# Performance work log

Measured on AMD Instinct MI355X. Metric: run time of the kernel, lower is better.

The kernel has to match this reference:

```python
import jax, jax.numpy as jnp
import numpy as np

# DeepseekV2MOE config (DeepSeek-V2-Lite-like, scaled)
T, H, E, I, K = 1024, 1024, 64, 512, 6
G, TKG = 8, 3          # n_group, topk_group
N_SHARED = 2
C = 256
SCALE = 2.5            # routed_scaling_factor


def setup_inputs() -> dict:
    key = jax.random.key(0)
    ks = jax.random.split(key, 7)
    inv = lambda d: 1.0 / np.sqrt(d).astype(np.float32)
    return {
        "hidden_states": jax.random.normal(ks[0], (T, H), jnp.float32),
        "gate_w": jax.random.normal(ks[1], (H, E), jnp.float32) * inv(H),
        "e_bias": jax.random.normal(ks[2], (E,), jnp.float32) * 0.01,  # e_score_correction_bias (noaux_tc)
        "w_gate_up": jax.random.normal(ks[3], (E, H, 2 * I), jnp.float32) * inv(H),
        "w_down": jax.random.normal(ks[4], (E, I, H), jnp.float32) * inv(I),
        "ws_gate_up": jax.random.normal(ks[5], (H, 2 * I * N_SHARED), jnp.float32) * inv(H),
        "ws_down": jax.random.normal(ks[6], (I * N_SHARED, H), jnp.float32) * inv(I * N_SHARED),
    }


def _silu_and_mul(gu):
    g, u = jnp.split(gu, 2, axis=-1)
    return jax.nn.silu(g) * u


def _grouped_topk(logits, bias):
    # DeepSeek-V3 noaux_tc grouped top-k with sigmoid scoring.
    scores = jax.nn.sigmoid(logits)                              # [T,E] original scores
    s = scores + bias[None, :]                                   # bias-corrected scores for selection
    grp = s.reshape(-1, G, E // G)
    grp_score = jax.lax.top_k(grp, 2)[0].sum(-1)                 # [T,G] sum of top-2 per group
    gidx = jax.lax.top_k(grp_score, TKG)[1]                      # [T,TKG]
    t = jnp.arange(s.shape[0])[:, None]
    gmask = jnp.zeros_like(grp_score, dtype=bool).at[t, gidx].set(True)
    emask = jnp.repeat(gmask, E // G, axis=1)                    # [T,E]
    eidx = jax.lax.top_k(jnp.where(emask, s, -jnp.inf), K)[1]    # [T,K]
    w = jnp.take_along_axis(scores, eidx, axis=1)                # weights from original (un-biased) scores
    w = w / w.sum(-1, keepdims=True)                             # renormalize (norm_topk_prob)
    return w, eidx


def _fused_moe(x, w, eidx, w_gate_up, w_down):
    # capacity-based dispatch -> grouped GEMM -> gather/scale combine
    A = x.shape[0] * K
    ef = eidx.reshape(A)                                         # expert id per assignment
    oh = jax.nn.one_hot(ef, E, dtype=jnp.int32)                  # [A,E]
    pos = ((jnp.cumsum(oh, axis=0) - 1) * oh).sum(-1)            # slot of each assignment within its expert
    xr = jnp.repeat(x, K, axis=0)                                # [A,H]
    xe = jnp.zeros((E, C, x.shape[1]), x.dtype).at[ef, pos].set(xr, mode="drop")  # [E,C,H]
    act = _silu_and_mul(jnp.einsum("ech,ehf->ecf", xe, w_gate_up))                # [E,C,I]
    ye = jnp.einsum("eci,eih->ech", act, w_down)                                   # [E,C,H]
    keep = (pos < C).astype(x.dtype)[:, None]
    yf = ye[ef, jnp.minimum(pos, C - 1)] * keep                  # [A,H]
    return (yf.reshape(-1, K, x.shape[1]) * w[..., None]).sum(1)  # [T,H]


def reference(hidden_states, gate_w, e_bias, w_gate_up, w_down, ws_gate_up, ws_down):
    shared = _silu_and_mul(hidden_states @ ws_gate_up) @ ws_down   # shared experts MLP
    logits = hidden_states @ gate_w                                # router
    w, eidx = _grouped_topk(logits, e_bias)
    routed = _fused_moe(hidden_states, w, eidx, w_gate_up, w_down)
    return routed * SCALE + shared                                 # non-fp16 branch
```

## Files before the change

kernel.cpp:

```cpp
#include <hip/hip_runtime.h>
#include <math.h>

typedef __bf16 bf16;
typedef bf16 bf16x8 __attribute__((ext_vector_type(8)));
typedef float f32x4 __attribute__((ext_vector_type(4)));
typedef unsigned int u32;

#define T_DIM 1024
#define H_DIM 1024
#define E_NUM 64
#define I_DIM 512
#define KTOP 6
#define TKG 3
#define CAP 256
#define A_TOT (T_DIM * KTOP)
#define SCALE_F 2.5f

#define BMx 128
#define BNx 128
#define BKx 64

typedef const u32 __attribute__((address_space(1)))* gas_t;
typedef u32 __attribute__((address_space(3)))* las_t;
__device__ __forceinline__ void gld16(const void* g, void* l) {
  __builtin_amdgcn_global_load_lds((gas_t)(unsigned long long)g,
                                   (las_t)(u32)(unsigned long long)l, 16, 0, 0);
}

__device__ __forceinline__ int bswz(int n) {
  return ((n >> 2) ^ ((n & 3) << 1)) & 7;
}

__global__ __launch_bounds__(256) void cvt_bf16(const float* __restrict__ in,
                                                bf16* __restrict__ out) {
  int i = (blockIdx.x * 256 + threadIdx.x) * 4;
  float4 v = *(const float4*)(in + i);
  bf16 __align__(8) t[4] = {(bf16)v.x, (bf16)v.y, (bf16)v.z, (bf16)v.w};
  *(uint2*)(out + i) = *(const uint2*)t;
}

__global__ __launch_bounds__(256) void router_topk(const float* __restrict__ x,
                                                   const float* __restrict__ gw,
                                                   const float* __restrict__ bias,
                                                   int* __restrict__ topk_id,
                                                   float* __restrict__ topk_w) {
  __shared__ float part[4][64];
  const int t = blockIdx.x;
  const int tid = threadIdx.x;
  const int wave = tid >> 6, lane = tid & 63;
  const float* xr = x + (long)t * H_DIM + wave * 256;
  float acc = 0.f;
  for (int h = 0; h < 256; h += 4) {
    float4 xv = *(const float4*)(xr + h);
    int hh = wave * 256 + h;
    acc += xv.x * gw[(hh + 0) * E_NUM + lane];
    acc += xv.y * gw[(hh + 1) * E_NUM + lane];
    acc += xv.z * gw[(hh + 2) * E_NUM + lane];
    acc += xv.w * gw[(hh + 3) * E_NUM + lane];
  }
  part[wave][lane] = acc;
  __syncthreads();
  if (wave != 0) return;
  acc = part[0][lane] + part[1][lane] + part[2][lane] + part[3][lane];

  float score = 1.f / (1.f + __expf(-acc));
  float sel = score + bias[lane];

  float m1 = sel, m2 = -INFINITY;
  #pragma unroll
  for (int off = 1; off < 8; off <<= 1) {
    float o1 = __shfl_xor(m1, off);
    float o2 = __shfl_xor(m2, off);
    float mn = fminf(m1, o1);
    float alt = (m1 >= o1) ? m2 : o2;
    m1 = fmaxf(m1, o1);
    m2 = fmaxf(mn, alt);
  }
  float gscore = m1 + m2;

  const int my_g = lane >> 3;
  unsigned gmask = 0;
  float gv = ((lane & 7) == 0) ? gscore : -INFINITY;
  for (int r = 0; r < TKG; ++r) {
    float v = gv;
    int idx = my_g;
    #pragma unroll
    for (int off = 1; off < 64; off <<= 1) {
      float ov = __shfl_xor(v, off);
      int oi = __shfl_xor(idx, off);
      if (ov > v || (ov == v && oi < idx)) { v = ov; idx = oi; }
    }
    gmask |= 1u << idx;
    if (my_g == idx) gv = -INFINITY;
  }

  float cand = ((gmask >> my_g) & 1u) ? sel : -INFINITY;
  float wk[KTOP];
  int ik[KTOP];
  float wsum = 0.f;
  for (int r = 0; r < KTOP; ++r) {
    float v = cand;
    int idx = lane;
    #pragma unroll
    for (int off = 1; off < 64; off <<= 1) {
      float ov = __shfl_xor(v, off);
      int oi = __shfl_xor(idx, off);
      if (ov > v || (ov == v && oi < idx)) { v = ov; idx = oi; }
    }
    float w = __shfl(score, idx);
    wk[r] = w; ik[r] = idx; wsum += w;
    if (lane == idx) cand = -INFINITY;
  }
  if (lane == 0) {
    float inv = 1.f / wsum;
    #pragma unroll
    for (int r = 0; r < KTOP; ++r) {
      topk_id[t * KTOP + r] = ik[r];
      topk_w[t * KTOP + r] = wk[r] * inv;
    }
  }
}

__global__ __launch_bounds__(64) void dispatch(const int* __restrict__ topk_id,
                                               int* __restrict__ rowlist,
                                               int* __restrict__ slot_a,
                                               int* __restrict__ counts) {
  __shared__ int ids[A_TOT];
  const int e = blockIdx.x, lane = threadIdx.x;
  for (int i = lane; i < A_TOT; i += 64) ids[i] = topk_id[i];
  __syncthreads();
  int base = 0;
  for (int a0 = 0; a0 < A_TOT; a0 += 64) {
    int a = a0 + lane;
    bool m = (ids[a] == e);
    unsigned long long bal = __ballot(m);
    if (m) {
      int pos = base + __popcll(bal & ((1ull << lane) - 1ull));
      slot_a[a] = (pos < CAP) ? pos : -1;
      if (pos < CAP) rowlist[e * CAP + pos] = a;
    }
    base += __popcll(bal);
  }
  if (lane == 0) counts[e] = (base < CAP) ? base : CAP;
}


__global__ __launch_bounds__(256) void gemm_gu(
    const bf16* __restrict__ X, int x_ld,
    const int* __restrict__ rows, const int* __restrict__ counts, int n_rows_fixed,
    const float* __restrict__ W, long w_estride, int ldb, int u_off,
    bf16* __restrict__ act, int act_ld, long act_estride, int kdim) {
  __shared__ union {
    struct { bf16 A[BMx * BKx]; bf16 B[BNx * BKx]; } st;
    bf16 epi[BMx * 72];
  } sm;
  const int e = blockIdx.z;
  const int n_rows = counts ? counts[e] : n_rows_fixed;
  const int m0 = blockIdx.x * BMx;
  if (m0 >= n_rows) return;
  const int nb = blockIdx.y;
  const int tid = threadIdx.x;
  const int w = tid >> 6, lane = tid & 63;
  const int q = lane >> 4, l16 = lane & 15;
  const int m_off = (w & 1) * 64;

  const int srow = w * 32 + (lane >> 3);
  const int gchunk = (lane & 7) ^ (lane >> 3);
  const bf16* pA[4];
  #pragma unroll
  for (int j = 0; j < 4; ++j) {
    int tr = m0 + srow + j * 8;
    int grow;
    if (rows) grow = (tr < n_rows) ? (rows[e * CAP + tr] / KTOP) : 0;
    else grow = tr;
    pA[j] = X + (long)grow * x_ld + gchunk * 8;
  }
  bf16* ldsA = sm.st.A + w * 2048 + lane * 8;

  const int kc = tid >> 5;
  const int n0 = (tid & 31) * 4;
  const int gcol = (n0 < 64) ? (nb * 64 + n0) : (u_off + nb * 64 + (n0 - 64));
  const float* bcol = W + (long)e * w_estride + (long)kc * 8 * ldb + gcol;
  float4 bv[8];
  #pragma unroll
  for (int r = 0; r < 8; ++r) bv[r] = *(const float4*)(bcol + (long)r * ldb);

  f32x4 acc[4][4];
  #pragma unroll
  for (int i = 0; i < 4; ++i)
    #pragma unroll
    for (int j = 0; j < 4; ++j) acc[i][j] = (f32x4){0.f, 0.f, 0.f, 0.f};

  for (int k0 = 0; k0 < kdim; k0 += BKx) {
    #pragma unroll
    for (int j = 0; j < 4; ++j) {
      gld16(pA[j], ldsA + j * 512);
      pA[j] += BKx;
    }
    #pragma unroll
    for (int j = 0; j < 4; ++j) {
      bf16 __align__(16) t8[8];
      #pragma unroll
      for (int r = 0; r < 8; ++r) t8[r] = (bf16)((const float*)&bv[r])[j];
      int n = n0 + j;
      *(uint4*)(sm.st.B + n * BKx + ((kc ^ bswz(n)) * 8)) = *(const uint4*)t8;
    }
    if (k0 + BKx < kdim) {
      const float* bnext = bcol + (long)(k0 + BKx) * ldb;
      #pragma unroll
      for (int r = 0; r < 8; ++r) bv[r] = *(const float4*)(bnext + (long)r * ldb);
    }
    __syncthreads();
    #pragma unroll
    for (int kh = 0; kh < 2; ++kh) {
      bf16x8 a[4], b[4];
      const int co = ((kh * 4 + q) ^ (l16 & 7)) * 8;
      #pragma unroll
      for (int i = 0; i < 4; ++i)
        a[i] = *(const bf16x8*)(sm.st.A + (m_off + i * 16 + l16) * BKx + co);
      #pragma unroll
      for (int j = 0; j < 4; ++j) {
        int nf = (j >> 1) * 64 + (w >> 1) * 32 + (j & 1) * 16;
        int n = nf + l16;
        b[j] = *(const bf16x8*)(sm.st.B + n * BKx + (((kh * 4 + q) ^ bswz(n)) * 8));
      }
      #pragma unroll
      for (int i = 0; i < 4; ++i)
        #pragma unroll
        for (int j = 0; j < 4; ++j)
          acc[i][j] = __builtin_amdgcn_mfma_f32_16x16x32_bf16(a[i], b[j], acc[i][j], 0, 0, 0);
    }
    __syncthreads();
  }

  const int c_base = (w >> 1) * 32;
  #pragma unroll
  for (int i = 0; i < 4; ++i)
    #pragma unroll
    for (int j = 0; j < 2; ++j)
      #pragma unroll
      for (int r = 0; r < 4; ++r) {
        float g = acc[i][j][r], uu = acc[i][j + 2][r];
        float s = g / (1.f + __expf(-g));
        sm.epi[(m_off + i * 16 + q * 4 + r) * 72 + c_base + j * 16 + l16] = (bf16)(s * uu);
      }
  __syncthreads();
  #pragma unroll
  for (int p = 0; p < 4; ++p) {
    int row = p * 32 + (tid >> 3);
    int c0 = (tid & 7) * 8;
    uint4 v = *(const uint4*)(sm.epi + row * 72 + c0);
    *(uint4*)(act + (long)e * act_estride + (long)(m0 + row) * act_ld + nb * 64 + c0) = v;
  }
}

template <typename OutT>
__global__ __launch_bounds__(256) void gemm_dn(
    const bf16* __restrict__ Abase, long a_estride, int a_ld,
    const int* __restrict__ rowsO, const int* __restrict__ counts, int n_rows_fixed,
    const float* __restrict__ W, long w_estride, int ldb,
    OutT* __restrict__ Out, int out_ld, int kdim) {
  __shared__ union {
    struct { bf16 A[BMx * BKx]; bf16 B[BNx * BKx]; } st;
    bf16 epi[BMx * 136];
  } sm;
  const int e = blockIdx.z;
  const int n_rows = counts ? counts[e] : n_rows_fixed;
  const int m0 = blockIdx.x * BMx;
  if (m0 >= n_rows) return;
  const int nb = blockIdx.y;
  const int tid = threadIdx.x;
  const int w = tid >> 6, lane = tid & 63;
  const int q = lane >> 4, l16 = lane & 15;
  const int m_off = (w & 1) * 64;
  const int n_off = (w >> 1) * 64;

  const int srow = w * 32 + (lane >> 3);
  const int gchunk = (lane & 7) ^ (lane >> 3);
  const bf16* pA[4];
  #pragma unroll
  for (int j = 0; j < 4; ++j)
    pA[j] = Abase + (long)e * a_estride + (long)(m0 + srow + j * 8) * a_ld + gchunk * 8;
  bf16* ldsA = sm.st.A + w * 2048 + lane * 8;

  const int kc = tid >> 5;
  const int n0 = (tid & 31) * 4;
  const float* bcol = W + (long)e * w_estride + (long)kc * 8 * ldb + nb * BNx + n0;
  float4 bv[8];
  #pragma unroll
  for (int r = 0; r < 8; ++r) bv[r] = *(const float4*)(bcol + (long)r * ldb);

  f32x4 acc[4][4];
  #pragma unroll
  for (int i = 0; i < 4; ++i)
    #pragma unroll
    for (int j = 0; j < 4; ++j) acc[i][j] = (f32x4){0.f, 0.f, 0.f, 0.f};

  for (int k0 = 0; k0 < kdim; k0 += BKx) {
    #pragma unroll
    for (int j = 0; j < 4; ++j) {
      gld16(pA[j], ldsA + j * 512);
      pA[j] += BKx;
    }
    #pragma unroll
    for (int j = 0; j < 4; ++j) {
      bf16 __align__(16) t8[8];
      #pragma unroll
      for (int r = 0; r < 8; ++r) t8[r] = (bf16)((const float*)&bv[r])[j];
      int n = n0 + j;
      *(uint4*)(sm.st.B + n * BKx + ((kc ^ bswz(n)) * 8)) = *(const uint4*)t8;
    }
    if (k0 + BKx < kdim) {
      const float* bnext = bcol + (long)(k0 + BKx) * ldb;
      #pragma unroll
      for (int r = 0; r < 8; ++r) bv[r] = *(const float4*)(bnext + (long)r * ldb);
    }
    __syncthreads();
    #pragma unroll
    for (int kh = 0; kh < 2; ++kh) {
      bf16x8 a[4], b[4];
      const int co = ((kh * 4 + q) ^ (l16 & 7)) * 8;
      #pragma unroll
      for (int i = 0; i < 4; ++i)
        a[i] = *(const bf16x8*)(sm.st.A + (m_off + i * 16 + l16) * BKx + co);
      #pragma unroll
      for (int j = 0; j < 4; ++j) {
        int n = n_off + j * 16 + l16;
        b[j] = *(const bf16x8*)(sm.st.B + n * BKx + (((kh * 4 + q) ^ bswz(n)) * 8));
      }
      #pragma unroll
      for (int i = 0; i < 4; ++i)
        #pragma unroll
        for (int j = 0; j < 4; ++j)
          acc[i][j] = __builtin_amdgcn_mfma_f32_16x16x32_bf16(a[i], b[j], acc[i][j], 0, 0, 0);
    }
    __syncthreads();
  }

  if constexpr (sizeof(OutT) == 4) {
    #pragma unroll
    for (int i = 0; i < 4; ++i)
      #pragma unroll
      for (int j = 0; j < 4; ++j)
        #pragma unroll
        for (int r = 0; r < 4; ++r) {
          int row = m0 + m_off + i * 16 + q * 4 + r;
          Out[(long)row * out_ld + nb * BNx + n_off + j * 16 + l16] = acc[i][j][r];
        }
  } else {
    #pragma unroll
    for (int i = 0; i < 4; ++i)
      #pragma unroll
      for (int j = 0; j < 4; ++j)
        #pragma unroll
        for (int r = 0; r < 4; ++r)
          sm.epi[(m_off + i * 16 + q * 4 + r) * 136 + n_off + j * 16 + l16] = (bf16)acc[i][j][r];
    __syncthreads();
    #pragma unroll
    for (int p = 0; p < 8; ++p) {
      int row = p * 16 + (tid >> 4);
      int c0 = (tid & 15) * 8;
      if (m0 + row < n_rows) {
        long orow = rowsO ? (long)rowsO[e * CAP + m0 + row] : (long)(m0 + row);
        *(uint4*)((bf16*)Out + orow * out_ld + nb * BNx + c0) =
            *(const uint4*)(sm.epi + row * 136 + c0);
      }
    }
  }
}

__global__ __launch_bounds__(256) void combine(const float* __restrict__ tkw,
                                               const int* __restrict__ slot_a,
                                               const bf16* __restrict__ Ya,
                                               float* __restrict__ out) {
  const int t = blockIdx.x, tid = threadIdx.x;
  long o = (long)t * H_DIM + tid * 4;
  float4 v = *(float4*)(out + o);
  float a0 = v.x, a1 = v.y, a2 = v.z, a3 = v.w;
  #pragma unroll
  for (int k = 0; k < KTOP; ++k) {
    int a = t * KTOP + k;
    if (slot_a[a] >= 0) {
      float w = tkw[a] * SCALE_F;
      const bf16* yr = Ya + (long)a * H_DIM + tid * 4;
      uint2 yv = *(const uint2*)yr;
      bf16 __align__(8) yb[4];
      *(uint2*)yb = yv;
      a0 += w * (float)yb[0];
      a1 += w * (float)yb[1];
      a2 += w * (float)yb[2];
      a3 += w * (float)yb[3];
    }
  }
  *(float4*)(out + o) = make_float4(a0, a1, a2, a3);
}

extern "C" void kernel_launch(void* const* d_in, const int* in_sizes, int n_in,
                              void* d_out, int out_size, void* d_ws, size_t ws_size,
                              hipStream_t stream) {
  const float* x     = (const float*)d_in[0];
  const float* gw    = (const float*)d_in[1];
  const float* bias  = (const float*)d_in[2];
  const float* w_gu  = (const float*)d_in[3];
  const float* w_dn  = (const float*)d_in[4];
  const float* ws_gu = (const float*)d_in[5];
  const float* ws_dn = (const float*)d_in[6];
  float* out = (float*)d_out;
  char* ws = (char*)d_ws;

  bf16* xbf     = (bf16*)(ws + 0);
  bf16* acts    = (bf16*)(ws + 2097152);
  bf16* actr    = (bf16*)(ws + 4194304);
  bf16* Ya      = (bf16*)(ws + 20971520);
  int*  tki     = (int*)(ws + 33554432);
  float* tkw    = (float*)(ws + 33579008);
  int*  rowlist = (int*)(ws + 33603584);
  int*  slot_a  = (int*)(ws + 33669120);
  int*  counts  = (int*)(ws + 33693696);

  cvt_bf16<<<dim3((T_DIM * H_DIM) / 1024), dim3(256), 0, stream>>>(x, xbf);
  router_topk<<<dim3(T_DIM), dim3(256), 0, stream>>>(x, gw, bias, tki, tkw);
  dispatch<<<dim3(E_NUM), dim3(64), 0, stream>>>(tki, rowlist, slot_a, counts);

  gemm_gu<<<dim3(CAP / BMx, I_DIM / 64, E_NUM), dim3(256), 0, stream>>>(
      xbf, H_DIM, rowlist, counts, 0,
      w_gu, (long)H_DIM * 2 * I_DIM, 2 * I_DIM, I_DIM,
      actr, I_DIM, (long)CAP * I_DIM, H_DIM);

  gemm_gu<<<dim3(T_DIM / BMx, 1024 / 64, 1), dim3(256), 0, stream>>>(
      xbf, H_DIM, nullptr, nullptr, T_DIM,
      ws_gu, 0, 2048, 1024,
      acts, 1024, 0, H_DIM);

  gemm_dn<bf16><<<dim3(CAP / BMx, H_DIM / BNx, E_NUM), dim3(256), 0, stream>>>(
      actr, (long)CAP * I_DIM, I_DIM, rowlist, counts, 0,
      w_dn, (long)I_DIM * H_DIM, H_DIM,
      (bf16*)Ya, H_DIM, I_DIM);

  gemm_dn<float><<<dim3(T_DIM / BMx, H_DIM / BNx, 1), dim3(256), 0, stream>>>(
      acts, 0, 1024, nullptr, nullptr, T_DIM,
      ws_dn, 0, H_DIM,
      out, H_DIM, 1024);

  combine<<<dim3(T_DIM), dim3(256), 0, stream>>>(tkw, slot_a, Ya, out);
}
```

Baseline: 595.9 us.

## Double-buffer A tiles in LDS to overlap global loads with MFMA

Both expert GEMM kernels now keep two LDS buffers for the A tile. The first tile is prefetched before the loop, and the async global_load_lds for the next tile is issued right after the barrier, so it overlaps the current tile's MFMA work. This aims to hide global-to-LDS latency that was previously exposed each iteration. It doubles A-tile LDS usage, which may lower occupancy. It also moves the barrier ahead of the B prefetch.

```diff
diff --git a/kernel.cpp b/kernel.cpp
--- a/kernel.cpp
+++ b/kernel.cpp
@@ -19,6 +19,7 @@
 #define BMx 128
 #define BNx 128
 #define BKx 64
+#define ABUF (BMx * BKx)
 
 typedef const u32 __attribute__((address_space(1)))* gas_t;
 typedef u32 __attribute__((address_space(3)))* las_t;
@@ -151,7 +152,7 @@
     const float* __restrict__ W, long w_estride, int ldb, int u_off,
     bf16* __restrict__ act, int act_ld, long act_estride, int kdim) {
   __shared__ union {
-    struct { bf16 A[BMx * BKx]; bf16 B[BNx * BKx]; } st;
+    struct { bf16 A[2 * ABUF]; bf16 B[BNx * BKx]; } st;
     bf16 epi[BMx * 72];
   } sm;
   const int e = blockIdx.z;
@@ -185,18 +186,21 @@
   #pragma unroll
   for (int r = 0; r < 8; ++r) bv[r] = *(const float4*)(bcol + (long)r * ldb);
 
+  #pragma unroll
+  for (int j = 0; j < 4; ++j) {
+    gld16(pA[j], ldsA + j * 512);
+    pA[j] += BKx;
+  }
+
   f32x4 acc[4][4];
   #pragma unroll
   for (int i = 0; i < 4; ++i)
     #pragma unroll
     for (int j = 0; j < 4; ++j) acc[i][j] = (f32x4){0.f, 0.f, 0.f, 0.f};
 
-  for (int k0 = 0; k0 < kdim; k0 += BKx) {
-    #pragma unroll
-    for (int j = 0; j < 4; ++j) {
-      gld16(pA[j], ldsA + j * 512);
-      pA[j] += BKx;
-    }
+  const int niter = kdim / BKx;
+  for (int k = 0; k < niter; ++k) {
+    const int p = k & 1;
     #pragma unroll
     for (int j = 0; j < 4; ++j) {
       bf16 __align__(16) t8[8];
@@ -205,19 +209,26 @@
       int n = n0 + j;
       *(uint4*)(sm.st.B + n * BKx + ((kc ^ bswz(n)) * 8)) = *(const uint4*)t8;
     }
-    if (k0 + BKx < kdim) {
-      const float* bnext = bcol + (long)(k0 + BKx) * ldb;
+    __syncthreads();
+
+    if (k + 1 < niter) {
+      const float* bnext = bcol + (long)(k + 1) * BKx * ldb;
       #pragma unroll
       for (int r = 0; r < 8; ++r) bv[r] = *(const float4*)(bnext + (long)r * ldb);
-    }
-    __syncthreads();
+      #pragma unroll
+      for (int j = 0; j < 4; ++j) {
+        gld16(pA[j], ldsA + (1 - p) * ABUF + j * 512);
+        pA[j] += BKx;
+      }
+    }
+
     #pragma unroll
     for (int kh = 0; kh < 2; ++kh) {
       bf16x8 a[4], b[4];
       const int co = ((kh * 4 + q) ^ (l16 & 7)) * 8;
       #pragma unroll
       for (int i = 0; i < 4; ++i)
-        a[i] = *(const bf16x8*)(sm.st.A + (m_off + i * 16 + l16) * BKx + co);
+        a[i] = *(const bf16x8*)(sm.st.A + p * ABUF + (m_off + i * 16 + l16) * BKx + co);
       #pragma unroll
       for (int j = 0; j < 4; ++j) {
         int nf = (j >> 1) * 64 + (w >> 1) * 32 + (j & 1) * 16;
@@ -261,7 +272,7 @@
     const float* __restrict__ W, long w_estride, int ldb,
     OutT* __restrict__ Out, int out_ld, int kdim) {
   __shared__ union {
-    struct { bf16 A[BMx * BKx]; bf16 B[BNx * BKx]; } st;
+    struct { bf16 A[2 * ABUF]; bf16 B[BNx * BKx]; } st;
     bf16 epi[BMx * 136];
   } sm;
   const int e = blockIdx.z;
@@ -290,18 +301,21 @@
   #pragma unroll
   for (int r = 0; r < 8; ++r) bv[r] = *(const float4*)(bcol + (long)r * ldb);
 
+  #pragma unroll
+  for (int j = 0; j < 4; ++j) {
+    gld16(pA[j], ldsA + j * 512);
+    pA[j] += BKx;
+  }
+
   f32x4 acc[4][4];
   #pragma unroll
   for (int i = 0; i < 4; ++i)
     #pragma unroll
     for (int j = 0; j < 4; ++j) acc[i][j] = (f32x4){0.f, 0.f, 0.f, 0.f};
 
-  for (int k0 = 0; k0 < kdim; k0 += BKx) {
-    #pragma unroll
-    for (int j = 0; j < 4; ++j) {
-      gld16(pA[j], ldsA + j * 512);
-      pA[j] += BKx;
-    }
+  const int niter = kdim / BKx;
+  for (int k = 0; k < niter; ++k) {
+    const int p = k & 1;
     #pragma unroll
     for (int j = 0; j < 4; ++j) {
       bf16 __align__(16) t8[8];
@@ -310,19 +324,26 @@
       int n = n0 + j;
       *(uint4*)(sm.st.B + n * BKx + ((kc ^ bswz(n)) * 8)) = *(const uint4*)t8;
     }
-    if (k0 + BKx < kdim) {
-      const float* bnext = bcol + (long)(k0 + BKx) * ldb;
+    __syncthreads();
+
+    if (k + 1 < niter) {
+      const float* bnext = bcol + (long)(k + 1) * BKx * ldb;
       #pragma unroll
       for (int r = 0; r < 8; ++r) bv[r] = *(const float4*)(bnext + (long)r * ldb);
-    }
-    __syncthreads();
+      #pragma unroll
+      for (int j = 0; j < 4; ++j) {
+        gld16(pA[j], ldsA + (1 - p) * ABUF + j * 512);
+        pA[j] += BKx;
+      }
+    }
+
     #pragma unroll
     for (int kh = 0; kh < 2; ++kh) {
       bf16x8 a[4], b[4];
       const int co = ((kh * 4 + q) ^ (l16 & 7)) * 8;
       #pragma unroll
       for (int i = 0; i < 4; ++i)
-        a[i] = *(const bf16x8*)(sm.st.A + (m_off + i * 16 + l16) * BKx + co);
+        a[i] = *(const bf16x8*)(sm.st.A + p * ABUF + (m_off + i * 16 + l16) * BKx + co);
       #pragma unroll
       for (int j = 0; j < 4; ++j) {
         int n = n_off + j * 16 + l16;
```

Result: faster. 579.9 us (-2.7%).
